# Performance work log

Measured on AMD Instinct MI355X. Metric: run time of the kernel, lower is better.

The kernel has to match this reference:

```python
import jax, jax.numpy as jnp
import numpy as np

EPS = 1e-3  # keras BatchNormalization default epsilon

def _spatial_shift(x):
    # x: [B, T, N, C]; channel c is circularly rolled along N by (c % N)
    B, T, N, C = x.shape
    shifts = np.arange(C) % N                      # [C]
    pos = np.arange(N)[:, None]                    # [N,1]
    # tf.roll(shift=s) moves element j to (j+s) % N, i.e. out[j] = in[(j - s) % N]
    gather_idx = (pos - shifts[None, :]) % N       # [N, C]
    return x[:, :, gather_idx, np.arange(C)]       # advanced indexing -> [B,T,N,C]

def setup_inputs() -> dict:
    key = jax.random.key(0)
    k1, k2, k3 = jax.random.split(key, 3)
    B, T, N, C_in, F = 8, 64, 21, 128, 256
    x = jax.random.normal(k1, (B, T, N, C_in), dtype=jnp.float32)
    W = jax.random.normal(k2, (C_in, F), dtype=jnp.float32) * (1.0 / np.sqrt(C_in))
    b = jnp.zeros((F,), dtype=jnp.float32)
    gamma = jnp.ones((F,), dtype=jnp.float32)
    beta = jnp.zeros((F,), dtype=jnp.float32)
    return {"x": x, "W": W, "b": b, "gamma": gamma, "beta": beta}

def reference(x, W, b, gamma, beta):
    # per-channel circular shift along N
    xs = _spatial_shift(x)                               # [B,T,N,C]
    # 1x1 conv == matmul over channel dim
    y = jnp.einsum('btnc,cf->btnf', xs, W) + b           # [B,T,N,F]
    # BatchNormalization with training=True: batch statistics over B,T,N
    mean = jnp.mean(y, axis=(0, 1, 2))
    var = jnp.var(y, axis=(0, 1, 2))
    y = (y - mean) * jax.lax.rsqrt(var + EPS) * gamma + beta
    return jax.nn.relu(y)
```

## Files before the change

kernel.cpp:

```cpp
#include <hip/hip_runtime.h>
#include <stdint.h>


#define NPOS 21
#define CIN  128
#define FOUT 256
#define BT   512
#define M_TOTAL 10752
#define BN_EPS 1e-3f
#define AROW 136
#define WSFRAG 1024

typedef short v8s __attribute__((ext_vector_type(8)));
typedef float v4f __attribute__((ext_vector_type(4)));

__device__ __forceinline__ uint16_t f2bf_rne(float f) {
    uint32_t u = __builtin_bit_cast(uint32_t, f);
    u += 0x7FFFu + ((u >> 16) & 1u);
    return (uint16_t)(u >> 16);
}

__global__ __launch_bounds__(256) void k_prep(const float* __restrict__ W,
                                              float* __restrict__ ws)
{
    const int t = threadIdx.x;
    const int b = blockIdx.x;
    if (b < 2) ws[b * 256 + t] = 0.0f;

    const int q  = b * 256 + t;
    const int l  = q & 63;
    const int ks = (q >> 6) & 3;
    const int nt = q >> 8;
    const int kb = ks * 32 + (l >> 4) * 8;
    const int col = nt * 16 + (l & 15);
    uint32_t d[4];
    #pragma unroll
    for (int p = 0; p < 4; p++) {
        uint32_t lo = f2bf_rne(W[(size_t)(kb + 2 * p    ) * FOUT + col]);
        uint32_t hi = f2bf_rne(W[(size_t)(kb + 2 * p + 1) * FOUT + col]);
        d[p] = lo | (hi << 16);
    }
    ((uint4*)(ws + WSFRAG))[q] = make_uint4(d[0], d[1], d[2], d[3]);
}

__global__ __launch_bounds__(256) void k_conv(const float* __restrict__ x,
                                              float* __restrict__ y,
                                              float* ws)
{
    __shared__ uint16_t asB[32 * AROW];
    __shared__ float scL[128], sqL[128];

    const int bt = blockIdx.x >> 1;
    const int fh = blockIdx.x & 1;
    const int t  = threadIdx.x;

    for (int i = t; i < 704; i += 256) {
        int r  = 21 + (i >> 6);
        int c2 = (i & 63) << 1;
        *(uint32_t*)&asB[r * AROW + c2] = 0u;
    }
    const float* xin = x + (size_t)bt * (NPOS * CIN);
    for (int i = t; i < NPOS * CIN; i += 256) {
        float v = xin[i];
        int r = i >> 7;
        int c = i & (CIN - 1);
        int s = c % NPOS;
        int n = r + s; if (n >= NPOS) n -= NPOS;
        asB[n * AROW + c] = f2bf_rne(v);
    }

    const int w     = t >> 6;
    const int l     = t & 63;
    const int row16 = l & 15;
    const int koct  = l >> 4;

    const uint4* wsw = (const uint4*)(ws + WSFRAG);
    v8s bfr[2][4];
    #pragma unroll
    for (int nt = 0; nt < 2; nt++) {
        const int ntg = fh * 8 + w * 2 + nt;
        #pragma unroll
        for (int ks = 0; ks < 4; ks++) {
            uint4 u = wsw[(((ntg << 2) + ks) << 6) + l];
            bfr[nt][ks] = __builtin_bit_cast(v8s, u);
        }
    }
    __syncthreads();

    v4f acc[2][2];
    #pragma unroll
    for (int m = 0; m < 2; m++)
        #pragma unroll
        for (int nt = 0; nt < 2; nt++) acc[m][nt] = (v4f){0.f, 0.f, 0.f, 0.f};

    #pragma unroll
    for (int m = 0; m < 2; m++) {
        v8s afr[4];
        #pragma unroll
        for (int ks = 0; ks < 4; ks++)
            afr[ks] = *(const v8s*)&asB[(m * 16 + row16) * AROW + ks * 32 + koct * 8];
        #pragma unroll
        for (int ks = 0; ks < 4; ks++)
            #pragma unroll
            for (int nt = 0; nt < 2; nt++)
                acc[m][nt] = __builtin_amdgcn_mfma_f32_16x16x32_bf16(
                                 afr[ks], bfr[nt][ks], acc[m][nt], 0, 0, 0);
    }

    float* yout = y + (size_t)bt * (NPOS * FOUT) + fh * 128 + w * 32;
    #pragma unroll
    for (int nt = 0; nt < 2; nt++) {
        float s = 0.f, q = 0.f;
        #pragma unroll
        for (int m = 0; m < 2; m++)
            #pragma unroll
            for (int rg = 0; rg < 4; rg++) {
                float v = acc[m][nt][rg];
                s += v; q += v * v;
                int gr = m * 16 + koct * 4 + rg;
                if (gr < NPOS)
                    yout[(size_t)gr * FOUT + nt * 16 + row16] = v;
            }
        s += __shfl_xor(s, 16); s += __shfl_xor(s, 32);
        q += __shfl_xor(q, 16); q += __shfl_xor(q, 32);
        if (l < 16) {
            scL[w * 32 + nt * 16 + l] = s;
            sqL[w * 32 + nt * 16 + l] = q;
        }
    }
    __syncthreads();

    if (t < 128) atomicAdd(ws + fh * 128 + t, scL[t]);
    else         atomicAdd(ws + 256 + fh * 128 + (t - 128), sqL[t - 128]);
}

#define BN_BLOCKS 1344

__global__ __launch_bounds__(256) void k_bnapply(float* __restrict__ y,
                                                 const float* __restrict__ ws,
                                                 const float* __restrict__ gamma,
                                                 const float* __restrict__ beta)
{
    const int t  = threadIdx.x;
    const int fb = (t & 63) << 2;
    const float4 sm = *(const float4*)(ws + fb);
    const float4 sq = *(const float4*)(ws + FOUT + fb);
    const float4 gm = *(const float4*)(gamma + fb);
    const float4 be = *(const float4*)(beta + fb);
    const float invM = 1.0f / (float)M_TOTAL;

    float sc[4], bs[4];
    {
        float m0 = sm.x * invM, m1 = sm.y * invM, m2 = sm.z * invM, m3 = sm.w * invM;
        float v0 = fmaf(-m0, m0, sq.x * invM);
        float v1 = fmaf(-m1, m1, sq.y * invM);
        float v2 = fmaf(-m2, m2, sq.z * invM);
        float v3 = fmaf(-m3, m3, sq.w * invM);
        sc[0] = rsqrtf(v0 + BN_EPS) * gm.x;  bs[0] = be.x - m0 * sc[0];
        sc[1] = rsqrtf(v1 + BN_EPS) * gm.y;  bs[1] = be.y - m1 * sc[1];
        sc[2] = rsqrtf(v2 + BN_EPS) * gm.z;  bs[2] = be.z - m2 * sc[2];
        sc[3] = rsqrtf(v3 + BN_EPS) * gm.w;  bs[3] = be.w - m3 * sc[3];
    }

    float4* y4 = (float4*)y;
    #pragma unroll
    for (int it = 0; it < 2; it++) {
        int g = blockIdx.x * 512 + it * 256 + t;
        float4 v = y4[g];
        v.x = fmaxf(fmaf(v.x, sc[0], bs[0]), 0.0f);
        v.y = fmaxf(fmaf(v.y, sc[1], bs[1]), 0.0f);
        v.z = fmaxf(fmaf(v.z, sc[2], bs[2]), 0.0f);
        v.w = fmaxf(fmaf(v.w, sc[3], bs[3]), 0.0f);
        y4[g] = v;
    }
}

extern "C" __global__ void SpatialShiftConvBlock_71923522339050_kernel() {}

extern "C" void kernel_launch(void* const* d_in, const int* in_sizes, int n_in,
                              void* d_out, int out_size, void* d_ws, size_t ws_size,
                              hipStream_t stream) {
    float* y  = (float*)d_out;
    float* ws = (float*)d_ws;
    k_prep<<<16, 256, 0, stream>>>((const float*)d_in[1], ws);
    k_conv<<<2 * BT, 256, 0, stream>>>((const float*)d_in[0], y, ws);
    k_bnapply<<<BN_BLOCKS, 256, 0, stream>>>(y, ws,
                                             (const float*)d_in[3], (const float*)d_in[4]);
}
```

Baseline: 91.41 us.

## Compute all output features per block and spread BN stat atomics over partitions

Each conv block now computes all 256 output features for one (b,t) slice instead of half, so the shifted, bf16-converted input tile is built once rather than twice. Launch count halves and per-wave MFMA work doubles, at the cost of more registers for weight fragments and accumulators. Batch-statistic atomics are spread across 8 partitions to reduce contention on the same addresses, and the BN apply kernel sums the partitions before use. k_prep now zeroes the larger statistics region.

```diff
diff --git a/kernel.cpp b/kernel.cpp
--- a/kernel.cpp
+++ b/kernel.cpp
@@ -9,7 +9,8 @@
 #define M_TOTAL 10752
 #define BN_EPS 1e-3f
 #define AROW 136
-#define WSFRAG 1024
+#define PARTS 8
+#define WSFRAG 4096
 
 typedef short v8s __attribute__((ext_vector_type(8)));
 typedef float v4f __attribute__((ext_vector_type(4)));
@@ -25,7 +26,7 @@
 {
     const int t = threadIdx.x;
     const int b = blockIdx.x;
-    if (b < 2) ws[b * 256 + t] = 0.0f;
+    ws[b * 256 + t] = 0.0f;
 
     const int q  = b * 256 + t;
     const int l  = q & 63;
@@ -48,10 +49,9 @@
                                               float* ws)
 {
     __shared__ uint16_t asB[32 * AROW];
-    __shared__ float scL[128], sqL[128];
+    __shared__ float sumL[FOUT], sqL[FOUT];
 
-    const int bt = blockIdx.x >> 1;
-    const int fh = blockIdx.x & 1;
+    const int bt = blockIdx.x;
     const int t  = threadIdx.x;
 
     for (int i = t; i < 704; i += 256) {
@@ -75,23 +75,21 @@
     const int koct  = l >> 4;
 
     const uint4* wsw = (const uint4*)(ws + WSFRAG);
-    v8s bfr[2][4];
+    v8s bfr[4][4];
     #pragma unroll
-    for (int nt = 0; nt < 2; nt++) {
-        const int ntg = fh * 8 + w * 2 + nt;
+    for (int nt = 0; nt < 4; nt++)
         #pragma unroll
         for (int ks = 0; ks < 4; ks++) {
-            uint4 u = wsw[(((ntg << 2) + ks) << 6) + l];
+            uint4 u = wsw[(((w * 4 + nt) * 4 + ks) << 6) + l];
             bfr[nt][ks] = __builtin_bit_cast(v8s, u);
         }
-    }
     __syncthreads();
 
-    v4f acc[2][2];
+    v4f acc[2][4];
     #pragma unroll
     for (int m = 0; m < 2; m++)
         #pragma unroll
-        for (int nt = 0; nt < 2; nt++) acc[m][nt] = (v4f){0.f, 0.f, 0.f, 0.f};
+        for (int nt = 0; nt < 4; nt++) acc[m][nt] = (v4f){0.f, 0.f, 0.f, 0.f};
 
     #pragma unroll
     for (int m = 0; m < 2; m++) {
@@ -102,14 +100,14 @@
         #pragma unroll
         for (int ks = 0; ks < 4; ks++)
             #pragma unroll
-            for (int nt = 0; nt < 2; nt++)
+            for (int nt = 0; nt < 4; nt++)
                 acc[m][nt] = __builtin_amdgcn_mfma_f32_16x16x32_bf16(
                                  afr[ks], bfr[nt][ks], acc[m][nt], 0, 0, 0);
     }
 
-    float* yout = y + (size_t)bt * (NPOS * FOUT) + fh * 128 + w * 32;
+    float* yout = y + (size_t)bt * (NPOS * FOUT) + w * 64;
     #pragma unroll
-    for (int nt = 0; nt < 2; nt++) {
+    for (int nt = 0; nt < 4; nt++) {
         float s = 0.f, q = 0.f;
         #pragma unroll
         for (int m = 0; m < 2; m++)
@@ -124,14 +122,15 @@
         s += __shfl_xor(s, 16); s += __shfl_xor(s, 32);
         q += __shfl_xor(q, 16); q += __shfl_xor(q, 32);
         if (l < 16) {
-            scL[w * 32 + nt * 16 + l] = s;
-            sqL[w * 32 + nt * 16 + l] = q;
+            sumL[w * 64 + nt * 16 + l] = s;
+            sqL [w * 64 + nt * 16 + l] = q;
         }
     }
     __syncthreads();
 
-    if (t < 128) atomicAdd(ws + fh * 128 + t, scL[t]);
-    else         atomicAdd(ws + 256 + fh * 128 + (t - 128), sqL[t - 128]);
+    float* part = ws + (bt & (PARTS - 1)) * 512;
+    atomicAdd(part + t, sumL[t]);
+    atomicAdd(part + 256 + t, sqL[t]);
 }
 
 #define BN_BLOCKS 1344
@@ -143,8 +142,15 @@
 {
     const int t  = threadIdx.x;
     const int fb = (t & 63) << 2;
-    const float4 sm = *(const float4*)(ws + fb);
-    const float4 sq = *(const float4*)(ws + FOUT + fb);
+    float4 sm = make_float4(0.f, 0.f, 0.f, 0.f);
+    float4 sq = make_float4(0.f, 0.f, 0.f, 0.f);
+    #pragma unroll
+    for (int p = 0; p < PARTS; p++) {
+        float4 a = *(const float4*)(ws + p * 512 + fb);
+        float4 b = *(const float4*)(ws + p * 512 + 256 + fb);
+        sm.x += a.x; sm.y += a.y; sm.z += a.z; sm.w += a.w;
+        sq.x += b.x; sq.y += b.y; sq.z += b.z; sq.w += b.w;
+    }
     const float4 gm = *(const float4*)(gamma + fb);
     const float4 be = *(const float4*)(beta + fb);
     const float invM = 1.0f / (float)M_TOTAL;
@@ -183,7 +189,7 @@
     float* y  = (float*)d_out;
     float* ws = (float*)d_ws;
     k_prep<<<16, 256, 0, stream>>>((const float*)d_in[1], ws);
-    k_conv<<<2 * BT, 256, 0, stream>>>((const float*)d_in[0], y, ws);
+    k_conv<<<BT, 256, 0, stream>>>((const float*)d_in[0], y, ws);
     k_bnapply<<<BN_BLOCKS, 256, 0, stream>>>(y, ws,
                                              (const float*)d_in[3], (const float*)d_in[4]);
 }
```

Result: faster. 82.49 us (-9.8%).
